# Kernel tuning notes

Measured on AMD Instinct MI355X. Metric: run time of the kernel, lower is better.

## Reference

```python
import jax, jax.numpy as jnp
import numpy as np

DIM = 512
HEADS = 8
HEAD_DIM = DIM // HEADS
MLP_HIDDEN = int(DIM * 4.0)
B, N = 4, 2048
LS_INIT = 1e-5
EPS = 1e-5


def _layernorm(x, w, b):
    mu = jnp.mean(x, axis=-1, keepdims=True)
    var = jnp.mean(jnp.square(x - mu), axis=-1, keepdims=True)
    return (x - mu) * jax.lax.rsqrt(var + EPS) * w + b


def setup_inputs() -> dict:
    key = jax.random.key(0)
    ks = jax.random.split(key, 12)
    s = 0.02
    return {
        "x": jax.random.normal(ks[0], (B, N, DIM), jnp.float32),
        "rel_pos_bias": jax.random.normal(ks[1], (HEADS, N, N), jnp.float32),
        "qkv_w": jax.random.normal(ks[2], (DIM, 3 * DIM), jnp.float32) * s,
        "qkv_b": jnp.zeros((3 * DIM,), jnp.float32),
        "out_w": jax.random.normal(ks[3], (DIM, DIM), jnp.float32) * s,
        "out_b": jnp.zeros((DIM,), jnp.float32),
        "ln1_w": jnp.ones((DIM,), jnp.float32),
        "ln1_b": jnp.zeros((DIM,), jnp.float32),
        "ln2_w": jnp.ones((DIM,), jnp.float32),
        "ln2_b": jnp.zeros((DIM,), jnp.float32),
        "ffn_w1": jax.random.normal(ks[4], (DIM, MLP_HIDDEN), jnp.float32) * s,
        "ffn_b1": jnp.zeros((MLP_HIDDEN,), jnp.float32),
        "ffn_w2": jax.random.normal(ks[5], (MLP_HIDDEN, DIM), jnp.float32) * s,
        "ffn_b2": jnp.zeros((DIM,), jnp.float32),
        "gamma1": jnp.full((DIM,), LS_INIT, jnp.float32),
        "gamma2": jnp.full((DIM,), LS_INIT, jnp.float32),
    }


def reference(x, rel_pos_bias, qkv_w, qkv_b, out_w, out_b, ln1_w, ln1_b,
              ln2_w, ln2_b, ffn_w1, ffn_b1, ffn_w2, ffn_b2, gamma1, gamma2):
    # Pre-norm MHA with relative-position bias
    y = _layernorm(x, ln1_w, ln1_b)                       # [B,N,C]
    qkv = y @ qkv_w + qkv_b                               # [B,N,3C]
    qkv = qkv.reshape(B, N, 3, HEADS, HEAD_DIM)
    q = jnp.transpose(qkv[:, :, 0], (0, 2, 1, 3))         # [B,H,N,D]
    k = jnp.transpose(qkv[:, :, 1], (0, 2, 1, 3))
    v = jnp.transpose(qkv[:, :, 2], (0, 2, 1, 3))
    scale = 1.0 / np.sqrt(HEAD_DIM).astype(np.float32)
    attn = jnp.einsum("bhid,bhjd->bhij", q, k) * scale    # [B,H,N,N]
    attn = attn + rel_pos_bias[None]
    attn = jax.nn.softmax(attn, axis=-1)
    out = jnp.einsum("bhij,bhjd->bhid", attn, v)          # [B,H,N,D]
    out = jnp.transpose(out, (0, 2, 1, 3)).reshape(B, N, DIM)
    out = out @ out_w + out_b
    x = x + out * gamma1                                  # layer scale, no drop-path (eval)
    # FFN with exact GELU
    y2 = _layernorm(x, ln2_w, ln2_b)
    h = jax.nn.gelu(y2 @ ffn_w1 + ffn_b1, approximate=False)
    ffn_out = h @ ffn_w2 + ffn_b2
    x = x + ffn_out * gamma2
    return x
```

## Files before the change

### kernel.cpp

```cpp
#include <hip/hip_runtime.h>
#include <hip/hip_bf16.h>
#include <math.h>

#define SEQ 2048
#define BATCH 4
#define DM 512
#define NH 8
#define HD 64
#define HID 2048
#define ROWS (BATCH * SEQ)

typedef __attribute__((ext_vector_type(8))) short short8;
typedef __attribute__((ext_vector_type(4))) float f32x4;

__device__ __forceinline__ short f2bf(float f) {
    unsigned u = __float_as_uint(f);
    u += 0x7fff + ((u >> 16) & 1);
    return (short)(u >> 16);
}

__device__ __forceinline__ void gl2lds16(const void* g, void* l) {
    __builtin_amdgcn_global_load_lds(
        (const __attribute__((address_space(1))) void*)g,
        (__attribute__((address_space(3))) void*)l, 16, 0, 0);
}

__global__ __launch_bounds__(256) void tcast_all(
    const float* __restrict__ qkv_w, const float* __restrict__ out_w,
    const float* __restrict__ w1, const float* __restrict__ w2,
    short* __restrict__ o_qkv, short* __restrict__ o_out,
    short* __restrict__ o_w1, short* __restrict__ o_w2) {
    __shared__ float tile[32][33];
    int id = blockIdx.x;
    const float* W; short* O; int K, N;
    if (id < 768)       { W = qkv_w; O = o_qkv; K = 512;  N = 1536; }
    else if (id < 1024) { W = out_w; O = o_out; K = 512;  N = 512;  id -= 768; }
    else if (id < 2048) { W = w1;    O = o_w1;  K = 512;  N = 2048; id -= 1024; }
    else                { W = w2;    O = o_w2;  K = 2048; N = 512;  id -= 2048; }
    int tn = N / 32;
    int n0 = (id % tn) * 32, k0 = (id / tn) * 32;
    int tx = threadIdx.x, ty = threadIdx.y;
#pragma unroll
    for (int i = 0; i < 4; ++i)
        tile[ty + i * 8][tx] = W[(size_t)(k0 + ty + i * 8) * N + n0 + tx];
    __syncthreads();
#pragma unroll
    for (int i = 0; i < 4; ++i)
        O[(size_t)(n0 + ty + i * 8) * K + k0 + tx] = f2bf(tile[tx][ty + i * 8]);
}

__global__ __launch_bounds__(256) void ln_k(const float* __restrict__ X,
                                            const float* __restrict__ g,
                                            const float* __restrict__ bta,
                                            short* __restrict__ Y) {
    int t = threadIdx.x;
    int wv = t >> 6, ln = t & 63;
    size_t row = (size_t)blockIdx.x * 4 + wv;
    const float* xr = X + row * DM;
    float4 v0 = *(const float4*)(xr + ln * 4);
    float4 v1 = *(const float4*)(xr + 256 + ln * 4);
    float s = v0.x + v0.y + v0.z + v0.w + v1.x + v1.y + v1.z + v1.w;
    float q = v0.x * v0.x + v0.y * v0.y + v0.z * v0.z + v0.w * v0.w +
              v1.x * v1.x + v1.y * v1.y + v1.z * v1.z + v1.w * v1.w;
#pragma unroll
    for (int off = 1; off < 64; off <<= 1) {
        s += __shfl_xor(s, off);
        q += __shfl_xor(q, off);
    }
    float mean = s * (1.0f / 512.0f);
    float var = q * (1.0f / 512.0f) - mean * mean;
    float rstd = rsqrtf(var + 1e-5f);
    int c0 = ln * 4, c1 = 256 + ln * 4;
    ushort4 o0, o1;
    o0.x = (unsigned short)f2bf((v0.x - mean) * rstd * g[c0 + 0] + bta[c0 + 0]);
    o0.y = (unsigned short)f2bf((v0.y - mean) * rstd * g[c0 + 1] + bta[c0 + 1]);
    o0.z = (unsigned short)f2bf((v0.z - mean) * rstd * g[c0 + 2] + bta[c0 + 2]);
    o0.w = (unsigned short)f2bf((v0.w - mean) * rstd * g[c0 + 3] + bta[c0 + 3]);
    o1.x = (unsigned short)f2bf((v1.x - mean) * rstd * g[c1 + 0] + bta[c1 + 0]);
    o1.y = (unsigned short)f2bf((v1.y - mean) * rstd * g[c1 + 1] + bta[c1 + 1]);
    o1.z = (unsigned short)f2bf((v1.z - mean) * rstd * g[c1 + 2] + bta[c1 + 2]);
    o1.w = (unsigned short)f2bf((v1.w - mean) * rstd * g[c1 + 3] + bta[c1 + 3]);
    *(ushort4*)((unsigned short*)Y + row * DM + c0) = o0;
    *(ushort4*)((unsigned short*)Y + row * DM + c1) = o1;
}

template <int EPI, int TN>
__global__ __launch_bounds__(256) void gemm_bt(const short* __restrict__ A,
                                               const short* __restrict__ Bt,
                                               const float* __restrict__ bias,
                                               const float* __restrict__ gamma,
                                               const float* __restrict__ res,
                                               void* __restrict__ Cout,
                                               short* __restrict__ Cout2,
                                               int M, int N, int K) {
    constexpr int NI = TN / 32;
    __shared__ __attribute__((aligned(16))) short As0[128][32];
    __shared__ __attribute__((aligned(16))) short As1[128][32];
    __shared__ __attribute__((aligned(16))) short Bs0[TN][32];
    __shared__ __attribute__((aligned(16))) short Bs1[TN][32];
    int t = threadIdx.x;
    int w = t >> 6, ln = t & 63;
    int quad = ln >> 4, l15 = ln & 15;
    int n0 = blockIdx.x * TN, m0 = blockIdx.y * 128;
    int wm = (w & 1) * 64, wn = (w >> 1) * (TN / 2);

    int srow0 = w * 32 + (ln >> 2);
    int srow1 = srow0 + 16;
    int srowB = w * 16 + (ln >> 2);
    int schunk = (ln & 3) * 8;
    const short* Ag0 = A + (size_t)(m0 + srow0) * K + schunk;
    const short* Ag1 = A + (size_t)(m0 + srow1) * K + schunk;
    const short* Bg0 = Bt + (size_t)(n0 + srow0) * K + schunk;
    const short* Bg1 = Bt + (size_t)(n0 + srow1) * K + schunk;
    const short* BgB = Bt + (size_t)(n0 + srowB) * K + schunk;

    f32x4 acc[4][NI];
#pragma unroll
    for (int i = 0; i < 4; ++i)
#pragma unroll
        for (int j = 0; j < NI; ++j) acc[i][j] = (f32x4){0.f, 0.f, 0.f, 0.f};

    for (int k0 = 0; k0 < K; k0 += 64) {
        __syncthreads();
        gl2lds16(Ag0 + k0, &As0[srow0][schunk]);
        gl2lds16(Ag1 + k0, &As0[srow1][schunk]);
        gl2lds16(Ag0 + k0 + 32, &As1[srow0][schunk]);
        gl2lds16(Ag1 + k0 + 32, &As1[srow1][schunk]);
        if (TN == 128) {
            gl2lds16(Bg0 + k0, &Bs0[srow0 & (TN - 1)][schunk]);
            gl2lds16(Bg1 + k0, &Bs0[srow1 & (TN - 1)][schunk]);
            gl2lds16(Bg0 + k0 + 32, &Bs1[srow0 & (TN - 1)][schunk]);
            gl2lds16(Bg1 + k0 + 32, &Bs1[srow1 & (TN - 1)][schunk]);
        } else {
            gl2lds16(BgB + k0, &Bs0[srowB & (TN - 1)][schunk]);
            gl2lds16(BgB + k0 + 32, &Bs1[srowB & (TN - 1)][schunk]);
        }
        __syncthreads();
        {
            short8 af[4], bf[NI];
#pragma unroll
            for (int mi = 0; mi < 4; ++mi)
                af[mi] = *(const short8*)&As0[wm + mi * 16 + l15][quad * 8];
#pragma unroll
            for (int ni = 0; ni < NI; ++ni)
                bf[ni] = *(const short8*)&Bs0[wn + ni * 16 + l15][quad * 8];
#pragma unroll
            for (int mi = 0; mi < 4; ++mi)
#pragma unroll
                for (int ni = 0; ni < NI; ++ni)
                    acc[mi][ni] = __builtin_amdgcn_mfma_f32_16x16x32_bf16(
                        af[mi], bf[ni], acc[mi][ni], 0, 0, 0);
        }
        {
            short8 af[4], bf[NI];
#pragma unroll
            for (int mi = 0; mi < 4; ++mi)
                af[mi] = *(const short8*)&As1[wm + mi * 16 + l15][quad * 8];
#pragma unroll
            for (int ni = 0; ni < NI; ++ni)
                bf[ni] = *(const short8*)&Bs1[wn + ni * 16 + l15][quad * 8];
#pragma unroll
            for (int mi = 0; mi < 4; ++mi)
#pragma unroll
                for (int ni = 0; ni < NI; ++ni)
                    acc[mi][ni] = __builtin_amdgcn_mfma_f32_16x16x32_bf16(
                        af[mi], bf[ni], acc[mi][ni], 0, 0, 0);
        }
    }

    if (EPI == 3 && n0 >= 1024) {
#pragma unroll
        for (int mi = 0; mi < 4; ++mi) {
#pragma unroll
            for (int ni = 0; ni < NI; ++ni) {
                int col = n0 + wn + ni * 16 + l15;
                int d = col - 1024, hh = d >> 6, dd = d & 63;
                int row0 = m0 + wm + mi * 16 + quad * 4;
                int bb = row0 >> 11, key = row0 & 2047;
                float bs = bias[col];
                ushort4 pk;
                pk.x = (unsigned short)f2bf(acc[mi][ni][0] + bs);
                pk.y = (unsigned short)f2bf(acc[mi][ni][1] + bs);
                pk.z = (unsigned short)f2bf(acc[mi][ni][2] + bs);
                pk.w = (unsigned short)f2bf(acc[mi][ni][3] + bs);
                *(ushort4*)&Cout2[((size_t)(bb * 8 + hh) * 64 + dd) * 2048 + key] = pk;
            }
        }
    } else {
#pragma unroll
        for (int mi = 0; mi < 4; ++mi) {
#pragma unroll
            for (int ni = 0; ni < NI; ++ni) {
#pragma unroll
                for (int r = 0; r < 4; ++r) {
                    int row = m0 + wm + mi * 16 + quad * 4 + r;
                    int col = n0 + wn + ni * 16 + l15;
                    float v = acc[mi][ni][r] + bias[col];
                    if (EPI == 0) {
                        ((short*)Cout)[(size_t)row * N + col] = f2bf(v);
                    } else if (EPI == 1) {
                        float u = v * fmaf(v * v, 0.0713548162f, 1.59576912f);
                        float gg = v / (1.0f + __expf(-u));
                        ((short*)Cout)[(size_t)row * N + col] = f2bf(gg);
                    } else if (EPI == 2) {
                        ((float*)Cout)[(size_t)row * N + col] =
                            fmaf(v, gamma[col], res[(size_t)row * N + col]);
                    } else {
                        float sc = (n0 < 512) ? 0.18033688f : 1.0f;
                        ((short*)Cout)[(size_t)row * 1024 + col] = f2bf(v * sc);
                    }
                }
            }
        }
    }
}

__global__ __launch_bounds__(256, 4) void attn_k(const short* __restrict__ qkv,
                                                 const short* __restrict__ vT,
                                                 const float* __restrict__ bias,
                                                 short* __restrict__ Aout) {
    __shared__ __attribute__((aligned(16))) short Ks[64 * 64];
    __shared__ __attribute__((aligned(16))) short Vs[64 * 64];
    __shared__ __attribute__((aligned(16))) short Ps[4][16 * 64];
    int t = threadIdx.x;
    int w = t >> 6, ln = t & 63, quad = ln >> 4, l15 = ln & 15;
    int idx = blockIdx.x;
    int h = idx & 7, b = (idx >> 3) & 3, qt = idx >> 5;
    int qb = qt * 64 + w * 16;
    const size_t cbase = (size_t)b * SEQ * 1024;

    const short* qrow = qkv + cbase + (size_t)(qb + l15) * 1024 + h * 64;
    short8 qf0 = *(const short8*)(qrow + quad * 8);
    short8 qf1 = *(const short8*)(qrow + 32 + quad * 8);

    int kr = t >> 3, kc = t & 7;
    const short* kg = qkv + cbase + 512 + h * 64 + kc * 8;
    const short* vg = vT + ((size_t)(b * 8 + h) * 64) * 2048 + kc * 8;
    int kswz = ((kc ^ (kr & 7)) * 8);
    int kd0 = kr * 64 + kswz;
    int kd1 = kd0 + 32 * 64;

    const float* bias_q = bias + (size_t)h * SEQ * SEQ +
                          (size_t)(qb + l15) * SEQ + quad * 4;

    short8 ones;
#pragma unroll
    for (int i = 0; i < 8; ++i) ones[i] = (short)0x3F80;

    f32x4 o[4], ol;
#pragma unroll
    for (int db = 0; db < 4; ++db) o[db] = (f32x4){0.f, 0.f, 0.f, 0.f};
    ol = (f32x4){0.f, 0.f, 0.f, 0.f};

    int sw7 = l15 & 7;

    float4 pk0 = *(const float4*)(kg + (size_t)kr * 1024);
    float4 pk1 = *(const float4*)(kg + (size_t)(kr + 32) * 1024);
    float4 pv0 = *(const float4*)(vg + (size_t)kr * 2048);
    float4 pv1 = *(const float4*)(vg + (size_t)(kr + 32) * 2048);
    float4 bbc[4];
#pragma unroll
    for (int ni = 0; ni < 4; ++ni)
        bbc[ni] = *(const float4*)(bias_q + ni * 16);

    for (int jt = 0; jt < 32; ++jt) {
        __syncthreads();
        *(float4*)&Ks[kd0] = pk0;
        *(float4*)&Ks[kd1] = pk1;
        *(float4*)&Vs[kd0] = pv0;
        *(float4*)&Vs[kd1] = pv1;
        __syncthreads();
        int j1 = (jt < 31) ? (jt + 1) * 64 : jt * 64;
        pk0 = *(const float4*)(kg + (size_t)(j1 + kr) * 1024);
        pk1 = *(const float4*)(kg + (size_t)(j1 + kr + 32) * 1024);
        pv0 = *(const float4*)(vg + (size_t)kr * 2048 + j1);
        pv1 = *(const float4*)(vg + (size_t)(kr + 32) * 2048 + j1);

        f32x4 s4[4];
#pragma unroll
        for (int ni = 0; ni < 4; ++ni) {
            short8 k0 = *(const short8*)&Ks[(ni * 16 + l15) * 64 + ((quad ^ sw7) * 8)];
            short8 k1 = *(const short8*)&Ks[(ni * 16 + l15) * 64 + (((4 + quad) ^ sw7) * 8)];
            s4[ni] = (f32x4){0.f, 0.f, 0.f, 0.f};
            s4[ni] = __builtin_amdgcn_mfma_f32_16x16x32_bf16(k0, qf0, s4[ni], 0, 0, 0);
            s4[ni] = __builtin_amdgcn_mfma_f32_16x16x32_bf16(k1, qf1, s4[ni], 0, 0, 0);
        }
#pragma unroll
        for (int ni = 0; ni < 4; ++ni) {
            float4 bb = bbc[ni];
            float2 plo, phi;
            plo.x = exp2f(fmaf(bb.x, 1.44269504f, s4[ni][0]));
            plo.y = exp2f(fmaf(bb.y, 1.44269504f, s4[ni][1]));
            phi.x = exp2f(fmaf(bb.z, 1.44269504f, s4[ni][2]));
            phi.y = exp2f(fmaf(bb.w, 1.44269504f, s4[ni][3]));
            bbc[ni] = *(const float4*)(bias_q + j1 + ni * 16);
            __hip_bfloat162 l2 = __float22bfloat162_rn(plo);
            __hip_bfloat162 h2 = __float22bfloat162_rn(phi);
            union { uint2 u; } pp;
            pp.u.x = *(unsigned*)&l2;
            pp.u.y = *(unsigned*)&h2;
            int c = ni * 2 + (quad >> 1);
            *(uint2*)&Ps[w][l15 * 64 + ((c ^ sw7) * 8) + (quad & 1) * 4] = pp.u;
        }
#pragma unroll
        for (int kk = 0; kk < 2; ++kk) {
            short8 ap = *(const short8*)&Ps[w][l15 * 64 + (((kk * 4 + quad) ^ sw7) * 8)];
#pragma unroll
            for (int db = 0; db < 4; ++db) {
                short8 vv = *(const short8*)&Vs[(db * 16 + l15) * 64 + (((kk * 4 + quad) ^ sw7) * 8)];
                o[db] = __builtin_amdgcn_mfma_f32_16x16x32_bf16(ap, vv, o[db], 0, 0, 0);
            }
            ol = __builtin_amdgcn_mfma_f32_16x16x32_bf16(ap, ones, ol, 0, 0, 0);
        }
    }
#pragma unroll
    for (int r = 0; r < 4; ++r) {
        float inv = 1.0f / ol[r];
        int qrow_g = b * SEQ + qb + quad * 4 + r;
#pragma unroll
        for (int db = 0; db < 4; ++db) {
            Aout[(size_t)qrow_g * DM + h * 64 + db * 16 + l15] =
                f2bf(o[db][r] * inv);
        }
    }
}

extern "C" void kernel_launch(void* const* d_in, const int* in_sizes, int n_in,
                              void* d_out, int out_size, void* d_ws, size_t ws_size,
                              hipStream_t stream) {
    const float* x      = (const float*)d_in[0];
    const float* bias   = (const float*)d_in[1];
    const float* qkv_w  = (const float*)d_in[2];
    const float* qkv_b  = (const float*)d_in[3];
    const float* out_w  = (const float*)d_in[4];
    const float* out_b  = (const float*)d_in[5];
    const float* ln1_w  = (const float*)d_in[6];
    const float* ln1_b  = (const float*)d_in[7];
    const float* ln2_w  = (const float*)d_in[8];
    const float* ln2_b  = (const float*)d_in[9];
    const float* ffn_w1 = (const float*)d_in[10];
    const float* ffn_b1 = (const float*)d_in[11];
    const float* ffn_w2 = (const float*)d_in[12];
    const float* ffn_b2 = (const float*)d_in[13];
    const float* gamma1 = (const float*)d_in[14];
    const float* gamma2 = (const float*)d_in[15];
    float* out = (float*)d_out;

    short* wqkvT = (short*)d_ws;
    short* woutT = wqkvT + (size_t)1536 * 512;
    short* w1T   = woutT + (size_t)512 * 512;
    short* w2T   = w1T + (size_t)2048 * 512;
    short* y1    = w2T + (size_t)512 * 2048;
    short* qkvB  = y1 + (size_t)ROWS * DM;
    short* vTb   = qkvB + (size_t)ROWS * 1024;
    short* aoutB = vTb + (size_t)32 * 64 * 2048;
    float* x1    = (float*)(aoutB + (size_t)ROWS * DM);
    short* hB    = qkvB;

    tcast_all<<<3072, dim3(32, 8), 0, stream>>>(qkv_w, out_w, ffn_w1, ffn_w2,
                                                wqkvT, woutT, w1T, w2T);
    ln_k<<<ROWS / 4, 256, 0, stream>>>(x, ln1_w, ln1_b, y1);
    gemm_bt<3, 128><<<dim3(1536 / 128, ROWS / 128), 256, 0, stream>>>(
        y1, wqkvT, qkv_b, nullptr, nullptr, qkvB, vTb, ROWS, 1536, 512);
    attn_k<<<1024, 256, 0, stream>>>(qkvB, vTb, bias, aoutB);
    gemm_bt<2, 64><<<dim3(512 / 64, ROWS / 128), 256, 0, stream>>>(
        aoutB, woutT, out_b, gamma1, x, x1, nullptr, ROWS, 512, 512);
    ln_k<<<ROWS / 4, 256, 0, stream>>>(x1, ln2_w, ln2_b, y1);
    gemm_bt<1, 128><<<dim3(2048 / 128, ROWS / 128), 256, 0, stream>>>(
        y1, w1T, ffn_b1, nullptr, nullptr, hB, nullptr, ROWS, 2048, 512);
    gemm_bt<2, 64><<<dim3(512 / 64, ROWS / 128), 256, 0, stream>>>(
        hB, w2T, ffn_b2, gamma2, x1, out, nullptr, ROWS, 512, 2048);
}
```

Baseline: 436.5 us.

## Split attention over two KV halves and merge partials in a combine kernel

The attention kernel now launches twice as many blocks, and each one processes half of the key/value sequence. It writes unnormalised fp32 partial outputs and row sums to workspace. A new combine kernel adds the two partials, normalises them, and writes the bf16 attention output. The intent is more parallelism and shorter per-block loops, at the cost of extra fp32 partial traffic and an additional kernel launch.

```diff
diff --git a/kernel.cpp b/kernel.cpp
--- a/kernel.cpp
+++ b/kernel.cpp
@@ -218,15 +218,21 @@
 __global__ __launch_bounds__(256, 4) void attn_k(const short* __restrict__ qkv,
                                                  const short* __restrict__ vT,
                                                  const float* __restrict__ bias,
-                                                 short* __restrict__ Aout) {
+                                                 float* __restrict__ O0,
+                                                 float* __restrict__ O1,
+                                                 float* __restrict__ lp) {
     __shared__ __attribute__((aligned(16))) short Ks[64 * 64];
     __shared__ __attribute__((aligned(16))) short Vs[64 * 64];
     __shared__ __attribute__((aligned(16))) short Ps[4][16 * 64];
     int t = threadIdx.x;
     int w = t >> 6, ln = t & 63, quad = ln >> 4, l15 = ln & 15;
     int idx = blockIdx.x;
-    int h = idx & 7, b = (idx >> 3) & 3, qt = idx >> 5;
+    int half = idx >> 10;
+    int rest = idx & 1023;
+    int h = rest & 7, b = (rest >> 3) & 3, qt = rest >> 5;
     int qb = qt * 64 + w * 16;
+    int jt0 = half * 16;
+    int j0 = jt0 * 64;
     const size_t cbase = (size_t)b * SEQ * 1024;
 
     const short* qrow = qkv + cbase + (size_t)(qb + l15) * 1024 + h * 64;
@@ -254,23 +260,23 @@
 
     int sw7 = l15 & 7;
 
-    float4 pk0 = *(const float4*)(kg + (size_t)kr * 1024);
-    float4 pk1 = *(const float4*)(kg + (size_t)(kr + 32) * 1024);
-    float4 pv0 = *(const float4*)(vg + (size_t)kr * 2048);
-    float4 pv1 = *(const float4*)(vg + (size_t)(kr + 32) * 2048);
+    float4 pk0 = *(const float4*)(kg + (size_t)(j0 + kr) * 1024);
+    float4 pk1 = *(const float4*)(kg + (size_t)(j0 + kr + 32) * 1024);
+    float4 pv0 = *(const float4*)(vg + (size_t)kr * 2048 + j0);
+    float4 pv1 = *(const float4*)(vg + (size_t)(kr + 32) * 2048 + j0);
     float4 bbc[4];
 #pragma unroll
     for (int ni = 0; ni < 4; ++ni)
-        bbc[ni] = *(const float4*)(bias_q + ni * 16);
-
-    for (int jt = 0; jt < 32; ++jt) {
+        bbc[ni] = *(const float4*)(bias_q + j0 + ni * 16);
+
+    for (int jt = jt0; jt < jt0 + 16; ++jt) {
         __syncthreads();
         *(float4*)&Ks[kd0] = pk0;
         *(float4*)&Ks[kd1] = pk1;
         *(float4*)&Vs[kd0] = pv0;
         *(float4*)&Vs[kd1] = pv1;
         __syncthreads();
-        int j1 = (jt < 31) ? (jt + 1) * 64 : jt * 64;
+        int j1 = (jt < jt0 + 15) ? (jt + 1) * 64 : jt * 64;
         pk0 = *(const float4*)(kg + (size_t)(j1 + kr) * 1024);
         pk1 = *(const float4*)(kg + (size_t)(j1 + kr + 32) * 1024);
         pv0 = *(const float4*)(vg + (size_t)kr * 2048 + j1);
@@ -313,16 +319,48 @@
             ol = __builtin_amdgcn_mfma_f32_16x16x32_bf16(ap, ones, ol, 0, 0, 0);
         }
     }
+    float* Od = half ? O1 : O0;
+    float* ld = lp + half * (32 * 2048);
 #pragma unroll
     for (int r = 0; r < 4; ++r) {
-        float inv = 1.0f / ol[r];
         int qrow_g = b * SEQ + qb + quad * 4 + r;
 #pragma unroll
         for (int db = 0; db < 4; ++db) {
-            Aout[(size_t)qrow_g * DM + h * 64 + db * 16 + l15] =
-                f2bf(o[db][r] * inv);
-        }
+            Od[(size_t)qrow_g * DM + h * 64 + db * 16 + l15] = o[db][r];
+        }
+        if (l15 == 0)
+            ld[(size_t)(b * 8 + h) * 2048 + qb + quad * 4 + r] = ol[r];
     }
+}
+
+__global__ __launch_bounds__(256) void comb_k(const float* __restrict__ O0,
+                                              const float* __restrict__ O1,
+                                              const float* __restrict__ lp,
+                                              short* __restrict__ Aout) {
+    int t = threadIdx.x;
+    int wv = t >> 6, ln = t & 63;
+    size_t row = (size_t)blockIdx.x * 4 + wv;
+    int b = (int)(row >> 11), q = (int)(row & 2047);
+    int h = ln >> 3;
+    float la = lp[(size_t)(b * 8 + h) * 2048 + q];
+    float lb = lp[32 * 2048 + (size_t)(b * 8 + h) * 2048 + q];
+    float inv = 1.0f / (la + lb);
+    const float* p0 = O0 + row * DM + ln * 8;
+    const float* p1 = O1 + row * DM + ln * 8;
+    float4 a0 = *(const float4*)p0;
+    float4 a1 = *(const float4*)(p0 + 4);
+    float4 c0 = *(const float4*)p1;
+    float4 c1 = *(const float4*)(p1 + 4);
+    short8 o;
+    o[0] = f2bf((a0.x + c0.x) * inv);
+    o[1] = f2bf((a0.y + c0.y) * inv);
+    o[2] = f2bf((a0.z + c0.z) * inv);
+    o[3] = f2bf((a0.w + c0.w) * inv);
+    o[4] = f2bf((a1.x + c1.x) * inv);
+    o[5] = f2bf((a1.y + c1.y) * inv);
+    o[6] = f2bf((a1.z + c1.z) * inv);
+    o[7] = f2bf((a1.w + c1.w) * inv);
+    *(short8*)(Aout + row * DM + ln * 8) = o;
 }
 
 extern "C" void kernel_launch(void* const* d_in, const int* in_sizes, int n_in,
@@ -355,6 +393,9 @@
     short* vTb   = qkvB + (size_t)ROWS * 1024;
     short* aoutB = vTb + (size_t)32 * 64 * 2048;
     float* x1    = (float*)(aoutB + (size_t)ROWS * DM);
+    float* opart1 = x1 + (size_t)ROWS * DM;
+    float* lpart  = opart1 + (size_t)ROWS * DM;
+    float* opart0 = x1;
     short* hB    = qkvB;
 
     tcast_all<<<3072, dim3(32, 8), 0, stream>>>(qkv_w, out_w, ffn_w1, ffn_w2,
@@ -362,7 +403,8 @@
     ln_k<<<ROWS / 4, 256, 0, stream>>>(x, ln1_w, ln1_b, y1);
     gemm_bt<3, 128><<<dim3(1536 / 128, ROWS / 128), 256, 0, stream>>>(
         y1, wqkvT, qkv_b, nullptr, nullptr, qkvB, vTb, ROWS, 1536, 512);
-    attn_k<<<1024, 256, 0, stream>>>(qkvB, vTb, bias, aoutB);
+    attn_k<<<2048, 256, 0, stream>>>(qkvB, vTb, bias, opart0, opart1, lpart);
+    comb_k<<<ROWS / 4, 256, 0, stream>>>(opart0, opart1, lpart, aoutB);
     gemm_bt<2, 64><<<dim3(512 / 64, ROWS / 128), 256, 0, stream>>>(
         aoutB, woutT, out_b, gamma1, x, x1, nullptr, ROWS, 512, 512);
     ln_k<<<ROWS / 4, 256, 0, stream>>>(x1, ln2_w, ln2_b, y1);
```

Result: slower. 446.0 us (+2.2%).
